# Optimization experiments

Measured on AMD Instinct MI355X. Metric: run time of the kernel, lower is better.

The kernel has to match this reference:

```python
import jax, jax.numpy as jnp
import numpy as np


def setup_inputs() -> dict:
    key = jax.random.key(0)
    k1, k2, k3 = jax.random.split(key, 3)
    B, N, T, F = 4, 512, 64, 256
    x = jax.random.normal(k1, (B, N, T, F), dtype=jnp.float32)
    adj = jax.random.uniform(k2, (N, N), dtype=jnp.float32)
    # nn.Linear(F, F, bias=False) weight, layout [out, in]
    theta_w = jax.random.normal(k3, (F, F), dtype=jnp.float32) / np.float32(np.sqrt(F))
    return {"x": x, "adj": adj, "theta_w": theta_w}


def reference(x, adj, theta_w):
    # x: (B, N, T, F) -> out: (B, N, T, F). Dropout p=0 (eval mode).
    B, N, T, F = x.shape
    scale = np.float32(1.0 / np.sqrt(F))
    # fold time into batch: (B*T, N, F)
    xf = jnp.transpose(x, (0, 2, 1, 3)).reshape(B * T, N, F)
    # SAt: softmax((x x^T)/sqrt(F)); forward divides by sqrt(F) again
    score = jnp.einsum("bnf,bmf->bnm", xf, xf) * scale
    att = jax.nn.softmax(score, axis=-1) * scale  # (B*T, N, N)
    # adjacency-masked attention aggregation
    h = jnp.einsum("bnm,bmf->bnf", adj[None, :, :] * att, xf)  # (B*T, N, F)
    # Theta linear (no bias): y = h @ W^T
    y = jnp.einsum("bnf,of->bno", h, theta_w)
    y = y.reshape(B, T, N, F).transpose(0, 2, 1, 3)  # (B, N, T, F)
    return jax.nn.relu(y)
```

## Files before the change

kernel.cpp:

```cpp
#include <hip/hip_runtime.h>


typedef __attribute__((ext_vector_type(8))) _Float16 h16x8;
typedef __attribute__((ext_vector_type(4))) float f32x4;
typedef __attribute__((ext_vector_type(4))) unsigned short us4;
typedef __attribute__((ext_vector_type(8))) unsigned short us8;

#define MFMA16(a, b, c) __builtin_amdgcn_mfma_f32_16x16x32_f16((a), (b), (c), 0, 0, 0)

__device__ __forceinline__ unsigned short f2h(float f) {
    _Float16 h = (_Float16)f;
    return __builtin_bit_cast(unsigned short, h);
}
__device__ __forceinline__ void st4(unsigned short* p, unsigned short a, unsigned short b,
                                    unsigned short c, unsigned short d) {
    us4 v = {a, b, c, d};
    *(us4*)p = v;
}
__device__ __forceinline__ us8 pack8(float4 a, float4 b) {
    us8 v = {f2h(a.x), f2h(a.y), f2h(a.z), f2h(a.w), f2h(b.x), f2h(b.y), f2h(b.z), f2h(b.w)};
    return v;
}
__device__ __forceinline__ void gload16(const void* g, void* l) {
    __builtin_amdgcn_global_load_lds(
        (const __attribute__((address_space(1))) unsigned int*)g,
        (__attribute__((address_space(3))) unsigned int*)l, 16, 0, 0);
}

namespace {
constexpr int Nn = 512;
constexpr int TT = 64;
constexpr int FF = 256;
constexpr int TTFF = TT * FF;
constexpr int PLD = 40;
constexpr int XLD = 264;
constexpr float SCALE = 0.0625f;
constexpr float K2 = 0.09016844f;
constexpr float C2 = 24.525816f;
constexpr float CLMP = 15.9f;
constexpr size_t XH_ELEMS = (size_t)256 * 512 * 256;
constexpr size_t XT_ELEMS = (size_t)256 * 256 * 512;
constexpr size_t WH_ELEMS = 256 * 256;
constexpr size_t AJ_ELEMS = (size_t)2 * 16 * 1024 * 8;
constexpr int KLD = 264;
constexpr int TLD = 72;
constexpr int FPLD = 40;
constexpr int HLD = 256;
constexpr int WLD = 128;
}

__global__ __launch_bounds__(256, 4) void prepass(const float* __restrict__ x,
                                                  const float* __restrict__ W,
                                                  const float* __restrict__ adj,
                                                  unsigned short* __restrict__ xh,
                                                  unsigned short* __restrict__ xT2,
                                                  unsigned short* __restrict__ Wh,
                                                  unsigned short* __restrict__ adjL) {
    const int bid = blockIdx.x;
    const int t = threadIdx.x;
    if (bid >= 2056) {
        const int bid2 = bid - 2056;
        #pragma unroll
        for (int k = 0; k < 4; ++k) {
            const int u = bid2 * 1024 + k * 256 + t;
            const int qh = u >> 14;
            const int t16 = (u >> 10) & 15;
            const int tv = u & 1023;
            const int wv = tv >> 6, lv = tv & 63, lgv = lv >> 4, lcv = lv & 15;
            us8 v;
            #pragma unroll
            for (int e = 0; e < 8; ++e) {
                const int jt = e >> 2, r = e & 3;
                v[e] = f2h(adj[(size_t)((qh << 8) + (wv << 4) + (lgv << 2) + r) * Nn +
                               (t16 << 5) + (jt << 4) + lcv]);
            }
            *(us8*)&adjL[(size_t)u * 8] = v;
        }
        return;
    }
    if (bid >= 2048) {
        const int j = (bid - 2048) * 256 + t;
        #pragma unroll
        for (int k = 0; k < 4; ++k) {
            float4 a = *(const float4*)(W + j * 32 + k * 8);
            float4 b = *(const float4*)(W + j * 32 + k * 8 + 4);
            *(us8*)&Wh[j * 32 + k * 8] = pack8(a, b);
        }
        return;
    }
    __shared__ unsigned short tile[64 * XLD];
    const int bt = bid >> 3;
    const int nc = bid & 7;
    const int b = bt >> 6, tt = bt & 63;
    const int nbase = nc * 64;
    const float* xbt = x + (size_t)b * (Nn * TTFF) + (size_t)tt * FF;

    const int fb8 = (t & 31) * 8;
    const int rg = t >> 5;
    #pragma unroll
    for (int i = 0; i < 8; ++i) {
        const int rl = rg * 8 + i;
        const int n = nbase + rl;
        float4 a = *(const float4*)(xbt + (size_t)n * TTFF + fb8);
        float4 c = *(const float4*)(xbt + (size_t)n * TTFF + fb8 + 4);
        us8 v = pack8(a, c);
        *(us8*)&xh[((size_t)bt * Nn + n) * FF + (fb8 ^ (8 * (n & 7)))] = v;
        *(us8*)&tile[rl * XLD + fb8] = v;
    }
    __syncthreads();
    const int n0 = (t & 7) * 8;
    const int fr = t >> 3;
    #pragma unroll
    for (int j = 0; j < 8; ++j) {
        const int f = fr + 32 * j;
        const int g2 = 8 * ((f >> 1) & 3);
        const int n0p = (n0 & 32) | ((n0 & 24) ^ g2);
        us8 v;
        #pragma unroll
        for (int k = 0; k < 8; ++k) v[k] = tile[(n0p + k) * XLD + f];
        const int m = nbase + n0;
        *(us8*)&xT2[((size_t)bt * 16 + (m >> 5)) * 8192 + f * 32 + (m & 31)] = v;
    }
}

__global__ __launch_bounds__(1024, 4) void gcn_main(float* __restrict__ out,
                                                    const unsigned short* __restrict__ xh,
                                                    const unsigned short* __restrict__ xT2,
                                                    const unsigned short* __restrict__ Wh,
                                                    const unsigned short* __restrict__ adjL) {
    __shared__ alignas(16) union {
        struct { unsigned short kt[2][32][256]; unsigned short vt[2][256][32];
                 unsigned short at[2][1024][8]; unsigned short pb[16][16][PLD]; } m;
        struct { unsigned short hb[256][264]; unsigned short wc[64][136]; } e;
    } sm;

    const int tid = threadIdx.x;
    const int w  = tid >> 6;
    const int l  = tid & 63;
    const int lg = l >> 4;
    const int lc = l & 15;
    const int fsw = 8 * (lc & 7);

    const int lb = (blockIdx.x & 7) * 64 + (blockIdx.x >> 3);
    const int bt = lb >> 1;
    const int qt = lb & 1;
    const int b  = bt >> 6;
    const int tt = bt & 63;
    const int qbase = qt * 256;

    const unsigned short* xhb = xh + (size_t)bt * (Nn * FF);
    const unsigned short* xTb = xT2 + (size_t)bt * (FF * Nn);
    const unsigned short* ajq = adjL + (size_t)qt * (16 * 1024 * 8);

    auto stage = [&](int u) {
        const int c = u & 1;
        const size_t off = (size_t)(u & 15) * 8192 + (size_t)tid * 8;
        gload16(&xhb[off], &sm.m.kt[c][0][0] + (size_t)tid * 8);
        gload16(&xTb[off], &sm.m.vt[c][0][0] + (size_t)tid * 8);
        gload16(&ajq[off], &sm.m.at[c][0][0] + (size_t)tid * 8);
    };

    stage(0);

    h16x8 qf[8];
    {
        const unsigned short* qp = &xhb[(size_t)(qbase + 16 * w + lc) * FF];
        #pragma unroll
        for (int ks = 0; ks < 8; ++ks) {
            us8 v = *(const us8*)(qp + ((ks * 32 + lg * 8) ^ fsw));
            qf[ks] = __builtin_bit_cast(h16x8, v);
        }
    }

    f32x4 acc[16];
    #pragma unroll
    for (int i = 0; i < 16; ++i) { f32x4 z = {0.f, 0.f, 0.f, 0.f}; acc[i] = z; }
    float rs[4] = {0.f, 0.f, 0.f, 0.f};
    const int msw2 = 8 * ((lc >> 1) & 3);

    for (int t = 0; t < 16; ++t) {
        const int c = t & 1;

        asm volatile("s_waitcnt vmcnt(0)" ::: "memory");
        __builtin_amdgcn_s_barrier();
        __builtin_amdgcn_sched_barrier(0);

        stage(t + 1);

        h16x8 arh = *(const h16x8*)&sm.m.at[c][tid][0];

        f32x4 s[2];
        #pragma unroll
        for (int jt = 0; jt < 2; ++jt) { f32x4 z = {0.f, 0.f, 0.f, 0.f}; s[jt] = z; }
        __builtin_amdgcn_s_setprio(1);
        #pragma unroll
        for (int ks = 0; ks < 8; ++ks) {
            const int col = (ks * 32 + lg * 8) ^ fsw;
            h16x8 b0 = *(const h16x8*)&sm.m.kt[c][lc][col];
            h16x8 b1 = *(const h16x8*)&sm.m.kt[c][16 + lc][col];
            s[0] = MFMA16(qf[ks], b0, s[0]);
            s[1] = MFMA16(qf[ks], b1, s[1]);
        }
        __builtin_amdgcn_s_setprio(0);

        #pragma unroll
        for (int jt = 0; jt < 2; ++jt)
            #pragma unroll
            for (int r = 0; r < 4; ++r) {
                float p = exp2f(fminf(fmaf(s[jt][r], K2, -C2), CLMP));
                rs[r] += p;
                float pp = p * (float)arh[jt * 4 + r];
                sm.m.pb[w][4 * lg + r][jt * 16 + lc] = f2h(pp);
            }
        h16x8 pa = *(const h16x8*)&sm.m.pb[w][lc][lg * 8];

        const int mcol = (lg * 8) ^ msw2;
        __builtin_amdgcn_s_setprio(1);
        #pragma unroll
        for (int ft = 0; ft < 16; ++ft) {
            h16x8 bv = *(const h16x8*)&sm.m.vt[c][ft * 16 + lc][mcol];
            acc[ft] = MFMA16(pa, bv, acc[ft]);
        }
        __builtin_amdgcn_s_setprio(0);
    }

    asm volatile("s_waitcnt vmcnt(0)" ::: "memory");
    __builtin_amdgcn_s_barrier();

    {
        float c0[4];
        #pragma unroll
        for (int r = 0; r < 4; ++r) {
            float t0 = rs[r];
            t0 += __shfl_xor(t0, 1);
            t0 += __shfl_xor(t0, 2);
            t0 += __shfl_xor(t0, 4);
            t0 += __shfl_xor(t0, 8);
            c0[r] = SCALE / t0;
        }
        #pragma unroll
        for (int ft = 0; ft < 16; ++ft)
            #pragma unroll
            for (int r = 0; r < 4; ++r)
                sm.e.hb[16 * w + 4 * lg + r][ft * 16 + lc] = f2h(acc[ft][r] * c0[r]);
    }

    const size_t outbase = ((size_t)(b * Nn + qbase + 16 * w + 4 * lg) * TT + tt) * FF;
    #pragma unroll
    for (int ohh = 0; ohh < 4; ++ohh) {
        f32x4 y4[4];
        #pragma unroll
        for (int i = 0; i < 4; ++i) { f32x4 z = {0.f, 0.f, 0.f, 0.f}; y4[i] = z; }
        #pragma unroll
        for (int fh = 0; fh < 2; ++fh) {
            __syncthreads();
            {
                const int o  = tid >> 4;
                const int cc = (tid & 15) * 8;
                *(us8*)&sm.e.wc[o][cc] =
                    *(const us8*)&Wh[(size_t)(ohh * 64 + o) * FF + fh * 128 + cc];
            }
            __syncthreads();
            h16x8 ha[4];
            #pragma unroll
            for (int k2 = 0; k2 < 4; ++k2)
                ha[k2] = *(const h16x8*)&sm.e.hb[16 * w + lc][fh * 128 + k2 * 32 + lg * 8];
            #pragma unroll
            for (int ot = 0; ot < 4; ++ot) {
                #pragma unroll
                for (int k2 = 0; k2 < 4; ++k2) {
                    h16x8 bw = *(const h16x8*)&sm.e.wc[ot * 16 + lc][k2 * 32 + lg * 8];
                    y4[ot] = MFMA16(ha[k2], bw, y4[ot]);
                }
            }
        }
        #pragma unroll
        for (int r = 0; r < 4; ++r) {
            float* op = &out[outbase + (size_t)r * (TT * FF)];
            #pragma unroll
            for (int ot = 0; ot < 4; ++ot) {
                const int o = ohh * 64 + ot * 16 + lc;
                float v = y4[ot][r];
                op[o] = v > 0.f ? v : 0.f;
            }
        }
    }
}

__global__ __launch_bounds__(256, 2) void gcn_fallback(const float* __restrict__ x,
                                                       const float* __restrict__ adj,
                                                       const float* __restrict__ W,
                                                       float* __restrict__ out) {
    __shared__ alignas(16) union {
        struct { unsigned short kt[64 * KLD]; unsigned short vt[256 * TLD];
                 unsigned short pb[4 * 32 * FPLD]; } m;
        struct { unsigned short hb[128 * HLD]; unsigned short wc[32 * WLD]; } e;
    } sm;

    const int tid = threadIdx.x;
    const int w  = tid >> 6;
    const int l  = tid & 63;
    const int lg = l >> 4;
    const int lc = l & 15;

    const int lb = (blockIdx.x & 7) * 128 + (blockIdx.x >> 3);
    const int bt = lb >> 2;
    const int qt = lb & 3;
    const int b  = bt >> 6;
    const int tt = bt & 63;
    const int qbase = qt * 128;

    const float* xbt = x + (size_t)b * (Nn * TTFF) + (size_t)tt * FF;

    h16x8 qf[2][8];
    #pragma unroll
    for (int qs = 0; qs < 2; ++qs) {
        const float* qp = xbt + (size_t)(qbase + 32 * w + 16 * qs + lc) * TTFF;
        #pragma unroll
        for (int ks = 0; ks < 8; ++ks) {
            float4 a = *(const float4*)(qp + ks * 32 + lg * 8);
            float4 c = *(const float4*)(qp + ks * 32 + lg * 8 + 4);
            h16x8 v;
            v[0] = (_Float16)(a.x * SCALE); v[1] = (_Float16)(a.y * SCALE);
            v[2] = (_Float16)(a.z * SCALE); v[3] = (_Float16)(a.w * SCALE);
            v[4] = (_Float16)(c.x * SCALE); v[5] = (_Float16)(c.y * SCALE);
            v[6] = (_Float16)(c.z * SCALE); v[7] = (_Float16)(c.w * SCALE);
            qf[qs][ks] = v;
        }
    }

    f32x4 acc[2][16];
    #pragma unroll
    for (int q = 0; q < 2; ++q)
        #pragma unroll
        for (int i = 0; i < 16; ++i) { f32x4 z = {0.f, 0.f, 0.f, 0.f}; acc[q][i] = z; }
    float mrow[2][4] = {{-1e30f,-1e30f,-1e30f,-1e30f},{-1e30f,-1e30f,-1e30f,-1e30f}};
    float lrow[2][4] = {{0.f,0.f,0.f,0.f},{0.f,0.f,0.f,0.f}};

    const int m0  = 4 * (tid >> 4);
    const int fb4 = 4 * (tid & 15);
    const int msw = m0 ^ (8 * (tid & 7));

    for (int kt2 = 0; kt2 < 8; ++kt2) {
        const int kbase = kt2 * 64;
        #pragma unroll
        for (int i = 0; i < 4; ++i) {
            const int f0 = fb4 + 64 * i;
            const float* p = xbt + (size_t)(kbase + m0) * TTFF + f0;
            float4 r0 = *(const float4*)(p);
            float4 r1 = *(const float4*)(p + TTFF);
            float4 r2 = *(const float4*)(p + 2 * TTFF);
            float4 r3 = *(const float4*)(p + 3 * TTFF);
            unsigned short a0=f2h(r0.x),a1=f2h(r0.y),a2=f2h(r0.z),a3=f2h(r0.w);
            unsigned short b0=f2h(r1.x),b1=f2h(r1.y),b2=f2h(r1.z),b3=f2h(r1.w);
            unsigned short c0=f2h(r2.x),c1=f2h(r2.y),c2=f2h(r2.z),c3=f2h(r2.w);
            unsigned short d0=f2h(r3.x),d1=f2h(r3.y),d2=f2h(r3.z),d3=f2h(r3.w);
            st4(&sm.m.kt[(m0 + 0) * KLD + f0], a0, a1, a2, a3);
            st4(&sm.m.kt[(m0 + 1) * KLD + f0], b0, b1, b2, b3);
            st4(&sm.m.kt[(m0 + 2) * KLD + f0], c0, c1, c2, c3);
            st4(&sm.m.kt[(m0 + 3) * KLD + f0], d0, d1, d2, d3);
            st4(&sm.m.vt[(f0 + 0) * TLD + msw], a0, b0, c0, d0);
            st4(&sm.m.vt[(f0 + 1) * TLD + msw], a1, b1, c1, d1);
            st4(&sm.m.vt[(f0 + 2) * TLD + msw], a2, b2, c2, d2);
            st4(&sm.m.vt[(f0 + 3) * TLD + msw], a3, b3, c3, d3);
        }
        __syncthreads();

        f32x4 s0[4], s1[4];
        #pragma unroll
        for (int jt = 0; jt < 4; ++jt) {
            f32x4 t0 = {0.f, 0.f, 0.f, 0.f}, t1 = {0.f, 0.f, 0.f, 0.f};
            #pragma unroll
            for (int ks = 0; ks < 8; ++ks) {
                h16x8 bf = *(const h16x8*)&sm.m.kt[(jt * 16 + lc) * KLD + ks * 32 + lg * 8];
                t0 = MFMA16(qf[0][ks], bf, t0);
                t1 = MFMA16(qf[1][ks], bf, t1);
            }
            s0[jt] = t0; s1[jt] = t1;
        }

        float resc[2][4];
        #pragma unroll
        for (int qs = 0; qs < 2; ++qs) {
            f32x4* s = qs ? s1 : s0;
            const int qrow0 = qbase + 32 * w + 16 * qs + 4 * lg;
            #pragma unroll
            for (int r = 0; r < 4; ++r) {
                float mx = fmaxf(fmaxf(s[0][r], s[1][r]), fmaxf(s[2][r], s[3][r]));
                mx = fmaxf(mx, __shfl_xor(mx, 1));
                mx = fmaxf(mx, __shfl_xor(mx, 2));
                mx = fmaxf(mx, __shfl_xor(mx, 4));
                mx = fmaxf(mx, __shfl_xor(mx, 8));
                float mnew = fmaxf(mrow[qs][r], mx);
                resc[qs][r] = exp2f((mrow[qs][r] - mnew) * 1.44269504f);
                mrow[qs][r] = mnew;
                float rss = 0.f;
                #pragma unroll
                for (int jt = 0; jt < 4; ++jt) {
                    float p = exp2f((s[jt][r] - mnew) * 1.44269504f);
                    rss += p;
                    s[jt][r] = p * adj[(qrow0 + r) * Nn + kbase + jt * 16 + lc];
                }
                rss += __shfl_xor(rss, 1);
                rss += __shfl_xor(rss, 2);
                rss += __shfl_xor(rss, 4);
                rss += __shfl_xor(rss, 8);
                lrow[qs][r] = lrow[qs][r] * resc[qs][r] + rss;
            }
        }
        #pragma unroll
        for (int qs = 0; qs < 2; ++qs)
            #pragma unroll
            for (int ft = 0; ft < 16; ++ft)
                #pragma unroll
                for (int r = 0; r < 4; ++r) acc[qs][ft][r] *= resc[qs][r];

        #pragma unroll
        for (int ks = 0; ks < 2; ++ks) {
            #pragma unroll
            for (int qs = 0; qs < 2; ++qs) {
                const f32x4* s = qs ? s1 : s0;
                #pragma unroll
                for (int jl = 0; jl < 2; ++jl)
                    #pragma unroll
                    for (int r = 0; r < 4; ++r)
                        sm.m.pb[(w * 32 + qs * 16 + 4 * lg + r) * FPLD + jl * 16 + lc] =
                            f2h(s[2 * ks + jl][r]);
            }
            h16x8 pa0 = *(const h16x8*)&sm.m.pb[(w * 32 + lc) * FPLD + lg * 8];
            h16x8 pa1 = *(const h16x8*)&sm.m.pb[(w * 32 + 16 + lc) * FPLD + lg * 8];
            #pragma unroll
            for (int ft = 0; ft < 16; ++ft) {
                const int f = ft * 16 + lc;
                const int ms = (ks * 32 + lg * 8) ^ (8 * ((4 * ft + (lc >> 2)) & 7));
                h16x8 bv = *(const h16x8*)&sm.m.vt[f * TLD + ms];
                acc[0][ft] = MFMA16(pa0, bv, acc[0][ft]);
                acc[1][ft] = MFMA16(pa1, bv, acc[1][ft]);
            }
        }
        __syncthreads();
    }

    {
        float c0[2][4];
        #pragma unroll
        for (int qs = 0; qs < 2; ++qs)
            #pragma unroll
            for (int r = 0; r < 4; ++r) c0[qs][r] = SCALE / lrow[qs][r];
        #pragma unroll
        for (int qs = 0; qs < 2; ++qs)
            #pragma unroll
            for (int ft = 0; ft < 16; ++ft)
                #pragma unroll
                for (int r = 0; r < 4; ++r) {
                    const int row = 32 * w + 16 * qs + 4 * lg + r;
                    const int col = (ft * 16 + lc) ^ (8 * ((4 * lg + r) & 7));
                    sm.e.hb[row * HLD + col] = f2h(acc[qs][ft][r] * c0[qs][r]);
                }
    }
    __syncthreads();

    f32x4 y[8][2][2];
    #pragma unroll
    for (int oh = 0; oh < 8; ++oh)
        #pragma unroll
        for (int qs = 0; qs < 2; ++qs)
            #pragma unroll
            for (int ot = 0; ot < 2; ++ot) { f32x4 z = {0.f,0.f,0.f,0.f}; y[oh][qs][ot] = z; }

    #pragma unroll
    for (int fh = 0; fh < 2; ++fh) {
        h16x8 ha[2][4];
        #pragma unroll
        for (int qs = 0; qs < 2; ++qs)
            #pragma unroll
            for (int k2 = 0; k2 < 4; ++k2) {
                const int row = 32 * w + 16 * qs + lc;
                const int col = (fh * 128 + k2 * 32 + lg * 8) ^ (8 * (lc & 7));
                ha[qs][k2] = *(const h16x8*)&sm.e.hb[row * HLD + col];
            }
        #pragma unroll
        for (int oh = 0; oh < 8; ++oh) {
            __syncthreads();
            {
                const int o  = tid >> 3;
                const int cb = (tid & 7) * 16;
                const float* gp = &W[(size_t)(oh * 32 + o) * FF + fh * 128 + cb];
                float4 v0 = *(const float4*)(gp);
                float4 v1 = *(const float4*)(gp + 4);
                float4 v2 = *(const float4*)(gp + 8);
                float4 v3 = *(const float4*)(gp + 12);
                const int sw = 16 * (o & 3);
                *(us8*)&sm.e.wc[o * WLD + (cb ^ sw)]       = pack8(v0, v1);
                *(us8*)&sm.e.wc[o * WLD + ((cb + 8) ^ sw)] = pack8(v2, v3);
            }
            __syncthreads();
            #pragma unroll
            for (int ot = 0; ot < 2; ++ot) {
                #pragma unroll
                for (int k2 = 0; k2 < 4; ++k2) {
                    const int row = ot * 16 + lc;
                    const int col = (k2 * 32 + lg * 8) ^ (16 * (lc & 3));
                    h16x8 bw = *(const h16x8*)&sm.e.wc[row * WLD + col];
                    y[oh][0][ot] = MFMA16(ha[0][k2], bw, y[oh][0][ot]);
                    y[oh][1][ot] = MFMA16(ha[1][k2], bw, y[oh][1][ot]);
                }
            }
        }
    }

    #pragma unroll
    for (int qs = 0; qs < 2; ++qs)
        #pragma unroll
        for (int r = 0; r < 4; ++r) {
            const int row = qbase + 32 * w + 16 * qs + 4 * lg + r;
            float* op = &out[((size_t)(b * Nn + row) * TT + tt) * FF];
            #pragma unroll
            for (int oh = 0; oh < 8; ++oh)
                #pragma unroll
                for (int ot = 0; ot < 2; ++ot) {
                    const int o = oh * 32 + ot * 16 + lc;
                    float v = y[oh][qs][ot][r];
                    op[o] = v > 0.f ? v : 0.f;
                }
        }
}

extern "C" void kernel_launch(void* const* d_in, const int* in_sizes, int n_in,
                              void* d_out, int out_size, void* d_ws, size_t ws_size,
                              hipStream_t stream) {
    const float* x   = (const float*)d_in[0];
    const float* adj = (const float*)d_in[1];
    const float* w   = (const float*)d_in[2];
    float* out       = (float*)d_out;
    (void)in_sizes; (void)n_in; (void)out_size;

    unsigned short* xh  = (unsigned short*)d_ws;
    unsigned short* xT2 = xh + XH_ELEMS;
    unsigned short* Wh  = xT2 + XT_ELEMS;
    unsigned short* aL  = Wh + WH_ELEMS;
    const size_t need = (XH_ELEMS + XT_ELEMS + WH_ELEMS + AJ_ELEMS) * sizeof(unsigned short);

    if (ws_size >= need) {
        prepass<<<dim3(2088), dim3(256), 0, stream>>>(x, w, adj, xh, xT2, Wh, aL);
        gcn_main<<<dim3(512), dim3(1024), 0, stream>>>(out, xh, xT2, Wh, aL);
    } else {
        gcn_fallback<<<dim3(1024), dim3(256), 0, stream>>>(x, adj, w, out);
    }
}
```

Measured before the change: 206.3 us.

## Halve main kernel block to 8 waves, each handling 32 query rows

Cuts the gcn_main block from 16 waves to 8, with each wave now computing two 16-row query sub-tiles. Each K/V fragment read from LDS then feeds two MFMAs, so LDS read traffic per FLOP drops. The adjacency prepass layout, the staging loads (two 16-byte loads per thread) and the P-buffer swizzle are all changed to match. In exchange, per-thread register pressure roughly doubles (accumulators 2x16 f32x4) and fewer waves are resident to hide latency.

```diff
diff --git a/kernel.cpp b/kernel.cpp
--- a/kernel.cpp
+++ b/kernel.cpp
@@ -41,7 +41,7 @@
 constexpr size_t XH_ELEMS = (size_t)256 * 512 * 256;
 constexpr size_t XT_ELEMS = (size_t)256 * 256 * 512;
 constexpr size_t WH_ELEMS = 256 * 256;
-constexpr size_t AJ_ELEMS = (size_t)2 * 16 * 1024 * 8;
+constexpr size_t AJ_ELEMS = (size_t)2 * 16 * 8192;
 constexpr int KLD = 264;
 constexpr int TLD = 72;
 constexpr int FPLD = 40;
@@ -62,19 +62,23 @@
         const int bid2 = bid - 2056;
         #pragma unroll
         for (int k = 0; k < 4; ++k) {
-            const int u = bid2 * 1024 + k * 256 + t;
-            const int qh = u >> 14;
-            const int t16 = (u >> 10) & 15;
-            const int tv = u & 1023;
-            const int wv = tv >> 6, lv = tv & 63, lgv = lv >> 4, lcv = lv & 15;
+            const int U = bid2 * 1024 + k * 256 + t;
+            const int qt  = U >> 14;
+            const int t16 = (U >> 10) & 15;
+            const int u   = U & 1023;
+            const int half = u >> 9;
+            const int wv   = (u >> 6) & 7;
+            const int lv   = u & 63;
+            const int lgv  = lv >> 4, lcv = lv & 15;
             us8 v;
             #pragma unroll
-            for (int e = 0; e < 8; ++e) {
-                const int jt = e >> 2, r = e & 3;
-                v[e] = f2h(adj[(size_t)((qh << 8) + (wv << 4) + (lgv << 2) + r) * Nn +
-                               (t16 << 5) + (jt << 4) + lcv]);
-            }
-            *(us8*)&adjL[(size_t)u * 8] = v;
+            for (int ee = 0; ee < 8; ++ee) {
+                const int jt = ee >> 2, r = ee & 3;
+                const int row = qt * 256 + wv * 32 + half * 16 + lgv * 4 + r;
+                const int col = t16 * 32 + jt * 16 + lcv;
+                v[ee] = f2h(adj[(size_t)row * Nn + col]);
+            }
+            *(us8*)&adjL[(size_t)U * 8] = v;
         }
         return;
     }
@@ -123,14 +127,14 @@
     }
 }
 
-__global__ __launch_bounds__(1024, 4) void gcn_main(float* __restrict__ out,
-                                                    const unsigned short* __restrict__ xh,
-                                                    const unsigned short* __restrict__ xT2,
-                                                    const unsigned short* __restrict__ Wh,
-                                                    const unsigned short* __restrict__ adjL) {
+__global__ __launch_bounds__(512, 2) void gcn_main(float* __restrict__ out,
+                                                   const unsigned short* __restrict__ xh,
+                                                   const unsigned short* __restrict__ xT2,
+                                                   const unsigned short* __restrict__ Wh,
+                                                   const unsigned short* __restrict__ adjL) {
     __shared__ alignas(16) union {
         struct { unsigned short kt[2][32][256]; unsigned short vt[2][256][32];
-                 unsigned short at[2][1024][8]; unsigned short pb[16][16][PLD]; } m;
+                 unsigned short at[2][8192]; unsigned short pb[8][32][PLD]; } m;
         struct { unsigned short hb[256][264]; unsigned short wc[64][136]; } e;
     } sm;
 
@@ -150,33 +154,44 @@
 
     const unsigned short* xhb = xh + (size_t)bt * (Nn * FF);
     const unsigned short* xTb = xT2 + (size_t)bt * (FF * Nn);
-    const unsigned short* ajq = adjL + (size_t)qt * (16 * 1024 * 8);
+    const unsigned short* ajq = adjL + (size_t)qt * (16 * 8192);
 
     auto stage = [&](int u) {
         const int c = u & 1;
         const size_t off = (size_t)(u & 15) * 8192 + (size_t)tid * 8;
-        gload16(&xhb[off], &sm.m.kt[c][0][0] + (size_t)tid * 8);
-        gload16(&xTb[off], &sm.m.vt[c][0][0] + (size_t)tid * 8);
-        gload16(&ajq[off], &sm.m.at[c][0][0] + (size_t)tid * 8);
+        unsigned short* ktd = &sm.m.kt[c][0][0] + (size_t)tid * 8;
+        unsigned short* vtd = &sm.m.vt[c][0][0] + (size_t)tid * 8;
+        unsigned short* atd = &sm.m.at[c][0]    + (size_t)tid * 8;
+        gload16(&xhb[off],        ktd);
+        gload16(&xhb[off + 4096], ktd + 4096);
+        gload16(&xTb[off],        vtd);
+        gload16(&xTb[off + 4096], vtd + 4096);
+        gload16(&ajq[off],        atd);
+        gload16(&ajq[off + 4096], atd + 4096);
     };
 
     stage(0);
 
-    h16x8 qf[8];
-    {
-        const unsigned short* qp = &xhb[(size_t)(qbase + 16 * w + lc) * FF];
+    h16x8 qf[2][8];
+    #pragma unroll
+    for (int qs = 0; qs < 2; ++qs) {
+        const unsigned short* qp = &xhb[(size_t)(qbase + 32 * w + 16 * qs + lc) * FF];
         #pragma unroll
         for (int ks = 0; ks < 8; ++ks) {
             us8 v = *(const us8*)(qp + ((ks * 32 + lg * 8) ^ fsw));
-            qf[ks] = __builtin_bit_cast(h16x8, v);
-        }
-    }
-
-    f32x4 acc[16];
-    #pragma unroll
-    for (int i = 0; i < 16; ++i) { f32x4 z = {0.f, 0.f, 0.f, 0.f}; acc[i] = z; }
-    float rs[4] = {0.f, 0.f, 0.f, 0.f};
+            qf[qs][ks] = __builtin_bit_cast(h16x8, v);
+        }
+    }
+
+    f32x4 acc[2][16];
+    #pragma unroll
+    for (int q = 0; q < 2; ++q)
+        #pragma unroll
+        for (int i = 0; i < 16; ++i) { f32x4 z = {0.f, 0.f, 0.f, 0.f}; acc[q][i] = z; }
+    float rs[2][4] = {{0.f,0.f,0.f,0.f},{0.f,0.f,0.f,0.f}};
     const int msw2 = 8 * ((lc >> 1) & 3);
+    const int pwsw = 8 * ((lg >> 1) & 1);
+    const int prsw = 8 * ((lc >> 3) & 1);
 
     for (int t = 0; t < 16; ++t) {
         const int c = t & 1;
@@ -187,39 +202,48 @@
 
         stage(t + 1);
 
-        h16x8 arh = *(const h16x8*)&sm.m.at[c][tid][0];
-
-        f32x4 s[2];
-        #pragma unroll
-        for (int jt = 0; jt < 2; ++jt) { f32x4 z = {0.f, 0.f, 0.f, 0.f}; s[jt] = z; }
+        h16x8 a0 = *(const h16x8*)&sm.m.at[c][(w << 9) + l * 8];
+        h16x8 a1 = *(const h16x8*)&sm.m.at[c][4096 + (w << 9) + l * 8];
+
+        f32x4 s[2][2];
+        #pragma unroll
+        for (int qs = 0; qs < 2; ++qs)
+            #pragma unroll
+            for (int jt = 0; jt < 2; ++jt) { f32x4 z = {0.f,0.f,0.f,0.f}; s[qs][jt] = z; }
         __builtin_amdgcn_s_setprio(1);
         #pragma unroll
         for (int ks = 0; ks < 8; ++ks) {
             const int col = (ks * 32 + lg * 8) ^ fsw;
             h16x8 b0 = *(const h16x8*)&sm.m.kt[c][lc][col];
             h16x8 b1 = *(const h16x8*)&sm.m.kt[c][16 + lc][col];
-            s[0] = MFMA16(qf[ks], b0, s[0]);
-            s[1] = MFMA16(qf[ks], b1, s[1]);
+            s[0][0] = MFMA16(qf[0][ks], b0, s[0][0]);
+            s[0][1] = MFMA16(qf[0][ks], b1, s[0][1]);
+            s[1][0] = MFMA16(qf[1][ks], b0, s[1][0]);
+            s[1][1] = MFMA16(qf[1][ks], b1, s[1][1]);
         }
         __builtin_amdgcn_s_setprio(0);
 
         #pragma unroll
-        for (int jt = 0; jt < 2; ++jt)
-            #pragma unroll
-            for (int r = 0; r < 4; ++r) {
-                float p = exp2f(fminf(fmaf(s[jt][r], K2, -C2), CLMP));
-                rs[r] += p;
-                float pp = p * (float)arh[jt * 4 + r];
-                sm.m.pb[w][4 * lg + r][jt * 16 + lc] = f2h(pp);
-            }
-        h16x8 pa = *(const h16x8*)&sm.m.pb[w][lc][lg * 8];
+        for (int qs = 0; qs < 2; ++qs)
+            #pragma unroll
+            for (int jt = 0; jt < 2; ++jt)
+                #pragma unroll
+                for (int r = 0; r < 4; ++r) {
+                    float p = exp2f(fminf(fmaf(s[qs][jt][r], K2, -C2), CLMP));
+                    rs[qs][r] += p;
+                    float av = (float)(qs ? a1[jt * 4 + r] : a0[jt * 4 + r]);
+                    sm.m.pb[w][qs * 16 + 4 * lg + r][(jt * 16 + lc) ^ pwsw] = f2h(p * av);
+                }
+        h16x8 pa0 = *(const h16x8*)&sm.m.pb[w][lc][(lg * 8) ^ prsw];
+        h16x8 pa1 = *(const h16x8*)&sm.m.pb[w][16 + lc][(lg * 8) ^ prsw];
 
         const int mcol = (lg * 8) ^ msw2;
         __builtin_amdgcn_s_setprio(1);
         #pragma unroll
         for (int ft = 0; ft < 16; ++ft) {
             h16x8 bv = *(const h16x8*)&sm.m.vt[c][ft * 16 + lc][mcol];
-            acc[ft] = MFMA16(pa, bv, acc[ft]);
+            acc[0][ft] = MFMA16(pa0, bv, acc[0][ft]);
+            acc[1][ft] = MFMA16(pa1, bv, acc[1][ft]);
         }
         __builtin_amdgcn_s_setprio(0);
     }
@@ -228,62 +252,75 @@
     __builtin_amdgcn_s_barrier();
 
     {
-        float c0[4];
-        #pragma unroll
-        for (int r = 0; r < 4; ++r) {
-            float t0 = rs[r];
-            t0 += __shfl_xor(t0, 1);
-            t0 += __shfl_xor(t0, 2);
-            t0 += __shfl_xor(t0, 4);
-            t0 += __shfl_xor(t0, 8);
-            c0[r] = SCALE / t0;
-        }
-        #pragma unroll
-        for (int ft = 0; ft < 16; ++ft)
-            #pragma unroll
-            for (int r = 0; r < 4; ++r)
-                sm.e.hb[16 * w + 4 * lg + r][ft * 16 + lc] = f2h(acc[ft][r] * c0[r]);
-    }
-
-    const size_t outbase = ((size_t)(b * Nn + qbase + 16 * w + 4 * lg) * TT + tt) * FF;
+        #pragma unroll
+        for (int qs = 0; qs < 2; ++qs) {
+            float c0[4];
+            #pragma unroll
+            for (int r = 0; r < 4; ++r) {
+                float t0 = rs[qs][r];
+                t0 += __shfl_xor(t0, 1);
+                t0 += __shfl_xor(t0, 2);
+                t0 += __shfl_xor(t0, 4);
+                t0 += __shfl_xor(t0, 8);
+                c0[r] = SCALE / t0;
+            }
+            #pragma unroll
+            for (int ft = 0; ft < 16; ++ft)
+                #pragma unroll
+                for (int r = 0; r < 4; ++r)
+                    sm.e.hb[32 * w + 16 * qs + 4 * lg + r][ft * 16 + lc] =
+                        f2h(acc[qs][ft][r] * c0[r]);
+        }
+    }
+
     #pragma unroll
     for (int ohh = 0; ohh < 4; ++ohh) {
-        f32x4 y4[4];
-        #pragma unroll
-        for (int i = 0; i < 4; ++i) { f32x4 z = {0.f, 0.f, 0.f, 0.f}; y4[i] = z; }
+        f32x4 y4[2][4];
+        #pragma unroll
+        for (int qs = 0; qs < 2; ++qs)
+            #pragma unroll
+            for (int i = 0; i < 4; ++i) { f32x4 z = {0.f, 0.f, 0.f, 0.f}; y4[qs][i] = z; }
         #pragma unroll
         for (int fh = 0; fh < 2; ++fh) {
             __syncthreads();
             {
-                const int o  = tid >> 4;
-                const int cc = (tid & 15) * 8;
-                *(us8*)&sm.e.wc[o][cc] =
-                    *(const us8*)&Wh[(size_t)(ohh * 64 + o) * FF + fh * 128 + cc];
+                const int o  = tid >> 3;
+                const int cc = (tid & 7) * 16;
+                const unsigned short* gp = &Wh[(size_t)(ohh * 64 + o) * FF + fh * 128 + cc];
+                *(us8*)&sm.e.wc[o][cc]     = *(const us8*)gp;
+                *(us8*)&sm.e.wc[o][cc + 8] = *(const us8*)(gp + 8);
             }
             __syncthreads();
-            h16x8 ha[4];
-            #pragma unroll
-            for (int k2 = 0; k2 < 4; ++k2)
-                ha[k2] = *(const h16x8*)&sm.e.hb[16 * w + lc][fh * 128 + k2 * 32 + lg * 8];
+            h16x8 ha[2][4];
+            #pragma unroll
+            for (int qs = 0; qs < 2; ++qs)
+                #pragma unroll
+                for (int k2 = 0; k2 < 4; ++k2)
+                    ha[qs][k2] = *(const h16x8*)
+                        &sm.e.hb[32 * w + 16 * qs + lc][fh * 128 + k2 * 32 + lg * 8];
             #pragma unroll
             for (int ot = 0; ot < 4; ++ot) {
                 #pragma unroll
                 for (int k2 = 0; k2 < 4; ++k2) {
                     h16x8 bw = *(const h16x8*)&sm.e.wc[ot * 16 + lc][k2 * 32 + lg * 8];
-                    y4[ot] = MFMA16(ha[k2], bw, y4[ot]);
-                }
-            }
-        }
-        #pragma unroll
-        for (int r = 0; r < 4; ++r) {
-            float* op = &out[outbase + (size_t)r * (TT * FF)];
-            #pragma unroll
-            for (int ot = 0; ot < 4; ++ot) {
-                const int o = ohh * 64 + ot * 16 + lc;
-                float v = y4[ot][r];
-                op[o] = v > 0.f ? v : 0.f;
-            }
-        }
+                    y4[0][ot] = MFMA16(ha[0][k2], bw, y4[0][ot]);
+                    y4[1][ot] = MFMA16(ha[1][k2], bw, y4[1][ot]);
+                }
+            }
+        }
+        #pragma unroll
+        for (int qs = 0; qs < 2; ++qs)
+            #pragma unroll
+            for (int r = 0; r < 4; ++r) {
+                const int row = qbase + 32 * w + 16 * qs + 4 * lg + r;
+                float* op = &out[((size_t)(b * Nn + row) * TT + tt) * FF];
+                #pragma unroll
+                for (int ot = 0; ot < 4; ++ot) {
+                    const int o = ohh * 64 + ot * 16 + lc;
+                    float v = y4[qs][ot][r];
+                    op[o] = v > 0.f ? v : 0.f;
+                }
+            }
     }
 }
 
@@ -543,7 +580,7 @@
 
     if (ws_size >= need) {
         prepass<<<dim3(2088), dim3(256), 0, stream>>>(x, w, adj, xh, xT2, Wh, aL);
-        gcn_main<<<dim3(512), dim3(1024), 0, stream>>>(out, xh, xT2, Wh, aL);
+        gcn_main<<<dim3(512), dim3(512), 0, stream>>>(out, xh, xT2, Wh, aL);
     } else {
         gcn_fallback<<<dim3(1024), dim3(256), 0, stream>>>(x, adj, w, out);
     }
```

Result: faster. 176.0 us (median of 3 runs) (-14.7%).
